# Performance work log

Hardware: AMD Instinct MI355X
Metric: run time of the kernel (lower is better)

Reference implementation:

```python
import jax, jax.numpy as jnp
import numpy as np

CHANS = [512, 1024, 512, 256, 256, 256]
RES = [(38, 38), (19, 19), (10, 10), (5, 5), (3, 3), (1, 1)]
NB = [4, 6, 6, 6, 4, 4]  # 2 + 2*len(aspect_ratios) per level (SSD300)
NC = 80                   # num_classes (conf conv outputs NC+1 per box)
B = 8


def _conv3x3(x, w, b):
    # x: [B, C, H, W], w: [O, C, 3, 3], stride 1, padding 1 (SAME)
    y = jax.lax.conv_general_dilated(
        x, w, window_strides=(1, 1), padding='SAME',
        dimension_numbers=('NCHW', 'OIHW', 'NCHW'))
    return y + b[None, :, None, None]


def setup_inputs() -> dict:
    key = jax.random.key(0)
    ks = jax.random.split(key, 6 * 3)
    d = {}
    for i in range(6):
        C = CHANS[i]
        H, W = RES[i]
        nb = NB[i]
        k = ks[i * 3:(i + 1) * 3]
        d[f'x{i}'] = jax.random.normal(k[0], (B, C, H, W), jnp.float32)
        d[f'loc_w{i}'] = jax.random.normal(k[1], (nb * 4, C, 3, 3), jnp.float32) * 0.02
        d[f'loc_b{i}'] = jnp.zeros((nb * 4,), jnp.float32)
        d[f'conf_w{i}'] = jax.random.normal(k[2], (nb * (NC + 1), C, 3, 3), jnp.float32) * 0.02
        d[f'conf_b{i}'] = jnp.zeros((nb * (NC + 1),), jnp.float32)
    return d


def reference(x0, loc_w0, loc_b0, conf_w0, conf_b0,
              x1, loc_w1, loc_b1, conf_w1, conf_b1,
              x2, loc_w2, loc_b2, conf_w2, conf_b2,
              x3, loc_w3, loc_b3, conf_w3, conf_b3,
              x4, loc_w4, loc_b4, conf_w4, conf_b4,
              x5, loc_w5, loc_b5, conf_w5, conf_b5):
    xs = [x0, x1, x2, x3, x4, x5]
    lws = [loc_w0, loc_w1, loc_w2, loc_w3, loc_w4, loc_w5]
    lbs = [loc_b0, loc_b1, loc_b2, loc_b3, loc_b4, loc_b5]
    cws = [conf_w0, conf_w1, conf_w2, conf_w3, conf_w4, conf_w5]
    cbs = [conf_b0, conf_b1, conf_b2, conf_b3, conf_b4, conf_b5]
    locs, confs = [], []
    for x, lw, lb, cw, cb in zip(xs, lws, lbs, cws, cbs):
        b = x.shape[0]
        # loc(act).view(B, 4, -1).permute(0, 2, 1)
        loc = _conv3x3(x, lw, lb).reshape(b, 4, -1).transpose(0, 2, 1)
        # conf(act).view(B, NC+1, -1).permute(0, 2, 1)
        conf = _conv3x3(x, cw, cb).reshape(b, NC + 1, -1).transpose(0, 2, 1)
        locs.append(loc)
        confs.append(conf)
    pred_locs = jnp.concatenate(locs, axis=1)    # [B, 8732, 4]
    pred_labels = jnp.concatenate(confs, axis=1)  # [B, 8732, 81]
    return pred_locs, pred_labels
```

## Files before the change

kernel.cpp:

```cpp
#include <hip/hip_runtime.h>
#include <stdint.h>


#define NTH 256
#define ATOT 8732
#define LOCTOT 279424
#define QS 36
#define TOTOUT 5937760
#define MR 8

typedef short short8 __attribute__((ext_vector_type(8)));
typedef float f32x4 __attribute__((ext_vector_type(4)));

__device__ __forceinline__ unsigned short f2bf(float f) {
  unsigned u = __float_as_uint(f);
  u += 0x7fffu + ((u >> 16) & 1u);
  return (unsigned short)(u >> 16);
}

__device__ __forceinline__ void gload_lds16(const void* g, void* l) {
  __builtin_amdgcn_global_load_lds(
      (const __attribute__((address_space(1))) unsigned int*)g,
      (__attribute__((address_space(3))) unsigned int*)l, 16, 0, 0);
}

struct PXs { const float* x; unsigned short* xh; int C, HWp, ptiles, boff; };
struct PX { PXs s[6]; };

__global__ __launch_bounds__(NTH) void prep_x(PX P) {
  __shared__ float T[64][65];
  const int bid = blockIdx.x;
  int e = 0;
  #pragma unroll
  for (int i = 1; i < 6; ++i) if (bid >= P.s[i].boff) e = i;
  const PXs sp = P.s[e];
  const int local = bid - sp.boff;
  const int p64 = local % sp.ptiles;
  const int t2  = local / sp.ptiles;
  const int Cq  = sp.C >> 6;
  const int c64 = t2 % Cq;
  const int bb  = t2 / Cq;

  const int tid = threadIdx.x;
  const int p0 = p64 << 6;
  const float* xs = sp.x + (size_t)(bb * sp.C + (c64 << 6)) * sp.HWp;
  const int tx = tid & 63, ty = tid >> 6;
  const int p = p0 + tx;
  const bool pok = p < sp.HWp;
  #pragma unroll
  for (int j = 0; j < 16; ++j) {
    int c = ty + (j << 2);
    T[c][tx] = pok ? xs[(size_t)c * sp.HWp + p] : 0.f;
  }
  __syncthreads();
  const int pl = tid >> 2, cs = (tid & 3) << 4;
  const int pg = p0 + pl;
  if (pg < sp.HWp) {
    unsigned short* dst = sp.xh + ((size_t)bb * sp.HWp + pg) * sp.C + (c64 << 6) + cs;
    short8 v0, v1;
    #pragma unroll
    for (int j = 0; j < 8; ++j) {
      v0[j] = (short)f2bf(T[cs + j][pl]);
      v1[j] = (short)f2bf(T[cs + 8 + j][pl]);
    }
    *(short8*)dst = v0;
    *(short8*)(dst + 8) = v1;
  }
}

struct PWs { const float *lw, *cw; unsigned short* wp; int C, lC, Nloc, Ntot, Npad, Kp; size_t tbase; };
struct PW { PWs s[6]; };

__global__ __launch_bounds__(NTH) void prep_w(PW P) {
  const size_t g = (size_t)blockIdx.x * NTH + threadIdx.x;
  int e = 0;
  #pragma unroll
  for (int i = 1; i < 6; ++i) if (g >= P.s[i].tbase) e = i;
  const PWs sp = P.s[e];
  const size_t local = g - sp.tbase;
  const int ci = (int)(local & (size_t)(sp.C - 1));
  const int co = (int)(local >> sp.lC);
  if (co >= sp.Npad) return;
  unsigned short* dst = sp.wp + (size_t)co * sp.Kp + ci;
  if (co >= sp.Ntot) {
    #pragma unroll
    for (int r = 0; r < 9; ++r) dst[(size_t)r * sp.C] = 0;
    return;
  }
  const float* wr = (co < sp.Nloc)
      ? (sp.lw + ((size_t)co * sp.C + ci) * 9)
      : (sp.cw + ((size_t)(co - sp.Nloc) * sp.C + ci) * 9);
  float v[9];
  #pragma unroll
  for (int r = 0; r < 9; ++r) v[r] = wr[r];
  #pragma unroll
  for (int r = 0; r < 9; ++r) dst[(size_t)r * sp.C] = f2bf(v[r]);
}

struct SG {
  const unsigned short *xh, *wp;
  float* yb;
  int H, W, HWp, C, lCq, Cq, Kp, M, Npad, mtiles, lgS, boff;
};
struct AG { SG s[6]; const char* zeros; int gq, gr; };

__global__ __launch_bounds__(NTH) void mbox_gemm(AG P) {
  __shared__ __align__(16) unsigned short A_s[2][128 * 64];
  __shared__ __align__(16) unsigned short B_s[2][128 * 64];

  const int bid = blockIdx.x;
  const int xcd = bid & 7, sidx = bid >> 3;
  const int g = (xcd < P.gr) ? xcd * (P.gq + 1) + sidx
                             : P.gr * (P.gq + 1) + (xcd - P.gr) * P.gq + sidx;

  int e = 0;
  #pragma unroll
  for (int i = 1; i < 6; ++i) if (g >= P.s[i].boff) e = i;
  const SG sp = P.s[e];
  const int gl = g - sp.boff;
  const int ks = gl & ((1 << sp.lgS) - 1);
  const int t2 = gl >> sp.lgS;
  const int mtile = t2 % sp.mtiles;
  const int ntile = t2 / sp.mtiles;

  const int tid = threadIdx.x, lane = tid & 63, wv = tid >> 6;
  const int wm = wv >> 1, wn = wv & 1;
  const int swz = ((lane & 7) ^ (lane >> 3)) << 4;
  const int rsub = lane >> 3;

  int bA[4], hA[4], wA[4]; bool mok[4];
  #pragma unroll
  for (int i = 0; i < 4; ++i) {
    int row = (wv << 5) + (i << 3) + rsub;
    int mg = mtile * 128 + row;
    bool ok = mg < sp.M;
    int mc = ok ? mg : 0;
    int bb = mc / sp.HWp; int p = mc - bb * sp.HWp;
    int hh = p / sp.W;    int ww = p - hh * sp.W;
    bA[i] = bb; hA[i] = hh; wA[i] = ww; mok[i] = ok;
  }

  const int q0 = ks * QS, q1 = q0 + QS;

  const char* curB[4];
  #pragma unroll
  for (int i = 0; i < 4; ++i) {
    int row = (wv << 5) + (i << 3) + rsub;
    int nrow = ntile * 128 + row;
    curB[i] = (const char*)(sp.wp + (size_t)nrow * sp.Kp + (size_t)q0 * 64) + swz;
  }

  const char* curA[4];
  auto setA = [&](int rr, int cq0) {
    int d3 = rr / 3; int dh = d3 - 1, dw = rr - d3 * 3 - 1;
    #pragma unroll
    for (int i = 0; i < 4; ++i) {
      int hh = hA[i] + dh, ww = wA[i] + dw;
      bool ok = mok[i] & ((unsigned)hh < (unsigned)sp.H) & ((unsigned)ww < (unsigned)sp.W);
      const unsigned short* base = ok
          ? sp.xh + (((size_t)bA[i] * sp.H + hh) * sp.W + ww) * sp.C + (cq0 << 6)
          : (const unsigned short*)P.zeros;
      curA[i] = (const char*)base + swz;
    }
  };

  auto stage = [&](int buf) {
    char* As = (char*)&A_s[buf][0];
    char* Bs = (char*)&B_s[buf][0];
    #pragma unroll
    for (int i = 0; i < 4; ++i)
      gload_lds16(curA[i], As + ((wv << 5) + (i << 3)) * 128);
    #pragma unroll
    for (int i = 0; i < 4; ++i)
      gload_lds16(curB[i], Bs + ((wv << 5) + (i << 3)) * 128);
  };

  f32x4 acc[4][4] = {};
  const int l15 = lane & 15, lh = lane >> 4;

  setA(q0 >> sp.lCq, q0 & (sp.Cq - 1));
  stage(0);
  #pragma unroll
  for (int i = 0; i < 4; ++i) { curA[i] += 128; curB[i] += 128; }

  int cur = 0;
  for (int q = q0; q < q1; ++q) {
    __syncthreads();
    if (q + 1 < q1) {
      if (((q + 1) & (sp.Cq - 1)) == 0) setA((q + 1) >> sp.lCq, 0);
      stage(cur ^ 1);
      #pragma unroll
      for (int i = 0; i < 4; ++i) { curA[i] += 128; curB[i] += 128; }
    }
    const char* As = (const char*)&A_s[cur][0];
    const char* Bs = (const char*)&B_s[cur][0];
    #pragma unroll
    for (int kk = 0; kk < 2; ++kk) {
      const int klb = ((kk << 5) + (lh << 3)) << 1;
      short8 af[4], bv[4];
      #pragma unroll
      for (int mf = 0; mf < 4; ++mf) {
        int row = (wm << 6) + (mf << 4) + l15;
        af[mf] = *(const short8*)(As + row * 128 + (klb ^ ((row & 7) << 4)));
      }
      #pragma unroll
      for (int nf = 0; nf < 4; ++nf) {
        int row = (wn << 6) + (nf << 4) + l15;
        bv[nf] = *(const short8*)(Bs + row * 128 + (klb ^ ((row & 7) << 4)));
      }
      #pragma unroll
      for (int mf = 0; mf < 4; ++mf)
        #pragma unroll
        for (int nf = 0; nf < 4; ++nf)
          acc[mf][nf] = __builtin_amdgcn_mfma_f32_16x16x32_bf16(af[mf], bv[nf], acc[mf][nf], 0, 0, 0);
    }
    cur ^= 1;
  }

  float* yb = sp.yb + (size_t)ks * sp.M * sp.Npad;
  #pragma unroll
  for (int nf = 0; nf < 4; ++nf) {
    const int ncol = ntile * 128 + (wn << 6) + (nf << 4) + l15;
    #pragma unroll
    for (int mf = 0; mf < 4; ++mf) {
      #pragma unroll
      for (int rg = 0; rg < 4; ++rg) {
        const int mg = mtile * 128 + (wm << 6) + (mf << 4) + (lh << 2) + rg;
        if (mg < sp.M) yb[(size_t)mg * sp.Npad + ncol] = acc[mf][nf][rg];
      }
    }
  }
}

struct SC2s { const float *yb, *lb, *cb; int HW, nb, S, Npad, M, abase, boff; };
struct SC2 { SC2s s[6]; };

__global__ __launch_bounds__(NTH) void mbox_scatter(SC2 P, float* __restrict__ out) {
  __shared__ float T[MR * 512];
  __shared__ float LB[32], CB[512];
  const int bid = blockIdx.x;
  int e = 0;
  #pragma unroll
  for (int i = 1; i < 6; ++i) if (bid >= P.s[i].boff) e = i;
  const SC2s sp = P.s[e];
  const int m0 = (bid - sp.boff) * MR;
  const int tid = threadIdx.x;
  const int HW = sp.HW, nb = sp.nb, Npad = sp.Npad;
  const int nb4v = nb * 4;

  for (int i = tid; i < nb4v; i += NTH) LB[i] = sp.lb[i];
  for (int i = tid; i < nb * 81; i += NTH) CB[i] = sp.cb[i];

  const int np4 = Npad >> 2;
  const int tot4 = MR * np4;
  const size_t dstride4 = (size_t)sp.M * np4;
  const float4* yb4 = (const float4*)sp.yb + (size_t)m0 * np4;
  float4* T4 = (float4*)T;
  for (int idx = tid; idx < tot4; idx += NTH) {
    const float4* p = yb4 + idx;
    float4 v = *p;
    for (int k = 1; k < sp.S; ++k) {
      p += dstride4;
      float4 w = *p;
      v.x += w.x; v.y += w.y; v.z += w.z; v.w += w.w;
    }
    T4[idx] = v;
  }
  __syncthreads();

  if (tid < MR * nb) {
    const int mloc = tid / nb, rb = tid - (tid / nb) * nb;
    const int m = m0 + mloc;
    const int b = m / HW, p = m - b * HW;
    const int aidx = sp.abase + rb * HW + p;
    float4 v;
    #pragma unroll
    for (int ii = 0; ii < 4; ++ii)
      (&v.x)[ii] = T[mloc * Npad + ii * nb + rb] + LB[ii * nb + rb];
    ((float4*)out)[(size_t)b * ATOT + aidx] = v;
  }

  const int totc = MR * nb * 81;
  float* outc = out + LOCTOT;
  for (int f = tid; f < totc; f += NTH) {
    const int ii = f % 81;
    const int gg = f / 81;
    const int rb = gg % nb;
    const int mloc = gg / nb;
    const int m = m0 + mloc;
    const int b = m / HW, p = m - b * HW;
    const int aidx = sp.abase + rb * HW + p;
    const int c = ii * nb + rb;
    outc[((size_t)b * ATOT + aidx) * 81 + ii] = T[mloc * Npad + nb4v + c] + CB[c];
  }
}

extern "C" void kernel_launch(void* const* d_in, const int* in_sizes, int n_in,
                              void* d_out, int out_size, void* d_ws, size_t ws_size,
                              hipStream_t stream) {
  static const int CH[6]  = {512, 1024, 512, 256, 256, 256};
  static const int HH[6]  = {38, 19, 10, 5, 3, 1};
  static const int NB_[6] = {4, 6, 6, 6, 4, 4};
  static const int SK[6]  = {2, 4, 2, 1, 1, 1};
  static const int LGS[6] = {1, 2, 1, 0, 0, 0};

  int abase[6]; { int a = 0; for (int s = 0; s < 6; ++s) { abase[s] = a; a += NB_[s] * HH[s] * HH[s]; } }

  size_t xh_off[6], wp_off[6], yb_off[6], off = 0;
  auto al = [](size_t v) { return (v + 255) & ~(size_t)255; };
  for (int s = 0; s < 6; ++s) { xh_off[s] = off; off = al(off + (size_t)8 * HH[s] * HH[s] * CH[s] * 2); }
  for (int s = 0; s < 6; ++s) {
    wp_off[s] = off;
    int Npad = ((NB_[s] * 85 + 127) / 128) * 128;
    off = al(off + (size_t)Npad * (CH[s] * 9) * 2);
  }
  const size_t zeros_off = off; off = al(off + 8192);
  for (int s = 0; s < 6; ++s) {
    yb_off[s] = off;
    int Npad = ((NB_[s] * 85 + 127) / 128) * 128;
    off = al(off + (size_t)SK[s] * (8 * HH[s] * HH[s]) * Npad * 4);
  }
  (void)ws_size;

  char* ws = (char*)d_ws;
  (void)hipMemsetAsync(ws + zeros_off, 0, 8192, stream);

  PX px; int pxb = 0;
  for (int s = 0; s < 6; ++s) {
    PXs& p = px.s[s];
    p.x = (const float*)d_in[5 * s + 0];
    p.xh = (unsigned short*)(ws + xh_off[s]);
    p.C = CH[s]; p.HWp = HH[s] * HH[s];
    p.ptiles = (p.HWp + 63) / 64;
    p.boff = pxb;
    pxb += 8 * (CH[s] >> 6) * p.ptiles;
  }
  hipLaunchKernelGGL(prep_x, dim3(pxb), dim3(NTH), 0, stream, px);

  PW pw; size_t tb = 0;
  for (int s = 0; s < 6; ++s) {
    PWs& p = pw.s[s];
    p.lw = (const float*)d_in[5 * s + 1];
    p.cw = (const float*)d_in[5 * s + 3];
    p.wp = (unsigned short*)(ws + wp_off[s]);
    p.C = CH[s];
    p.lC = (CH[s] == 1024) ? 10 : (CH[s] == 512 ? 9 : 8);
    p.Nloc = NB_[s] * 4; p.Ntot = NB_[s] * 85;
    p.Npad = ((p.Ntot + 127) / 128) * 128;
    p.Kp = CH[s] * 9;
    p.tbase = tb;
    tb += (size_t)p.Npad * CH[s];
  }
  hipLaunchKernelGGL(prep_w, dim3((unsigned)((tb + NTH - 1) / NTH)), dim3(NTH), 0, stream, pw);

  AG ag; ag.zeros = ws + zeros_off;
  int G = 0;
  for (int s = 0; s < 6; ++s) {
    SG& g = ag.s[s];
    g.xh = (const unsigned short*)(ws + xh_off[s]);
    g.wp = (const unsigned short*)(ws + wp_off[s]);
    g.yb = (float*)(ws + yb_off[s]);
    g.H = HH[s]; g.W = HH[s]; g.HWp = HH[s] * HH[s];
    g.C = CH[s];
    g.Cq = CH[s] >> 6;
    g.lCq = (g.Cq == 16) ? 4 : (g.Cq == 8 ? 3 : 2);
    g.Kp = CH[s] * 9;
    g.M = 8 * g.HWp;
    g.Npad = ((NB_[s] * 85 + 127) / 128) * 128;
    g.mtiles = (g.M + 127) / 128;
    g.lgS = LGS[s];
    g.boff = G;
    G += g.mtiles * (g.Npad >> 7) * SK[s];
  }
  ag.gq = G / 8; ag.gr = G % 8;
  hipLaunchKernelGGL(mbox_gemm, dim3(G), dim3(NTH), 0, stream, ag);

  SC2 sc; int SB = 0;
  for (int s = 0; s < 6; ++s) {
    SC2s& p = sc.s[s];
    p.yb = (const float*)(ws + yb_off[s]);
    p.lb = (const float*)d_in[5 * s + 2];
    p.cb = (const float*)d_in[5 * s + 4];
    p.HW = HH[s] * HH[s];
    p.nb = NB_[s];
    p.S = SK[s];
    p.Npad = ((NB_[s] * 85 + 127) / 128) * 128;
    p.M = 8 * p.HW;
    p.abase = abase[s];
    p.boff = SB;
    SB += p.M / MR;
  }
  hipLaunchKernelGGL(mbox_scatter, dim3(SB), dim3(NTH), 0, stream, sc, (float*)d_out);
}
```

Baseline: 148.3 us.

## Store GEMM split-K partials as bf16 and merge prep kernels into one launch

The GEMM now writes its split-K partial outputs as bf16 instead of fp32, halving the intermediate buffer traffic written by the GEMM and read back by the scatter kernel, which now sums bf16 partials in fp32. Separately, the activation-transpose and weight-repack prep kernels are fused into one launch that branches on block index, removing one kernel launch. The bf16 partials add rounding error to each split-K partial sum before the final reduction, which may affect output tolerance.

```diff
diff --git a/kernel.cpp b/kernel.cpp
--- a/kernel.cpp
+++ b/kernel.cpp
@@ -10,6 +10,7 @@
 #define MR 8
 
 typedef short short8 __attribute__((ext_vector_type(8)));
+typedef unsigned short ushort8 __attribute__((ext_vector_type(8)));
 typedef float f32x4 __attribute__((ext_vector_type(4)));
 
 __device__ __forceinline__ unsigned short f2bf(float f) {
@@ -18,6 +19,10 @@
   return (unsigned short)(u >> 16);
 }
 
+__device__ __forceinline__ float bf2f(unsigned short b) {
+  return __uint_as_float((unsigned)b << 16);
+}
+
 __device__ __forceinline__ void gload_lds16(const void* g, void* l) {
   __builtin_amdgcn_global_load_lds(
       (const __attribute__((address_space(1))) unsigned int*)g,
@@ -25,81 +30,79 @@
 }
 
 struct PXs { const float* x; unsigned short* xh; int C, HWp, ptiles, boff; };
-struct PX { PXs s[6]; };
-
-__global__ __launch_bounds__(NTH) void prep_x(PX P) {
+struct PWs { const float *lw, *cw; unsigned short* wp; int C, lC, Nloc, Ntot, Npad, Kp; size_t tbase; };
+struct PREP { PXs x[6]; PWs w[6]; int pxb; };
+
+__global__ __launch_bounds__(NTH) void prep_all(PREP P) {
   __shared__ float T[64][65];
-  const int bid = blockIdx.x;
-  int e = 0;
-  #pragma unroll
-  for (int i = 1; i < 6; ++i) if (bid >= P.s[i].boff) e = i;
-  const PXs sp = P.s[e];
-  const int local = bid - sp.boff;
-  const int p64 = local % sp.ptiles;
-  const int t2  = local / sp.ptiles;
-  const int Cq  = sp.C >> 6;
-  const int c64 = t2 % Cq;
-  const int bb  = t2 / Cq;
-
   const int tid = threadIdx.x;
-  const int p0 = p64 << 6;
-  const float* xs = sp.x + (size_t)(bb * sp.C + (c64 << 6)) * sp.HWp;
-  const int tx = tid & 63, ty = tid >> 6;
-  const int p = p0 + tx;
-  const bool pok = p < sp.HWp;
-  #pragma unroll
-  for (int j = 0; j < 16; ++j) {
-    int c = ty + (j << 2);
-    T[c][tx] = pok ? xs[(size_t)c * sp.HWp + p] : 0.f;
-  }
-  __syncthreads();
-  const int pl = tid >> 2, cs = (tid & 3) << 4;
-  const int pg = p0 + pl;
-  if (pg < sp.HWp) {
-    unsigned short* dst = sp.xh + ((size_t)bb * sp.HWp + pg) * sp.C + (c64 << 6) + cs;
-    short8 v0, v1;
-    #pragma unroll
-    for (int j = 0; j < 8; ++j) {
-      v0[j] = (short)f2bf(T[cs + j][pl]);
-      v1[j] = (short)f2bf(T[cs + 8 + j][pl]);
-    }
-    *(short8*)dst = v0;
-    *(short8*)(dst + 8) = v1;
-  }
-}
-
-struct PWs { const float *lw, *cw; unsigned short* wp; int C, lC, Nloc, Ntot, Npad, Kp; size_t tbase; };
-struct PW { PWs s[6]; };
-
-__global__ __launch_bounds__(NTH) void prep_w(PW P) {
-  const size_t g = (size_t)blockIdx.x * NTH + threadIdx.x;
-  int e = 0;
-  #pragma unroll
-  for (int i = 1; i < 6; ++i) if (g >= P.s[i].tbase) e = i;
-  const PWs sp = P.s[e];
-  const size_t local = g - sp.tbase;
-  const int ci = (int)(local & (size_t)(sp.C - 1));
-  const int co = (int)(local >> sp.lC);
-  if (co >= sp.Npad) return;
-  unsigned short* dst = sp.wp + (size_t)co * sp.Kp + ci;
-  if (co >= sp.Ntot) {
-    #pragma unroll
-    for (int r = 0; r < 9; ++r) dst[(size_t)r * sp.C] = 0;
-    return;
-  }
-  const float* wr = (co < sp.Nloc)
-      ? (sp.lw + ((size_t)co * sp.C + ci) * 9)
-      : (sp.cw + ((size_t)(co - sp.Nloc) * sp.C + ci) * 9);
-  float v[9];
-  #pragma unroll
-  for (int r = 0; r < 9; ++r) v[r] = wr[r];
-  #pragma unroll
-  for (int r = 0; r < 9; ++r) dst[(size_t)r * sp.C] = f2bf(v[r]);
+  if ((int)blockIdx.x < P.pxb) {
+    const int bid = blockIdx.x;
+    int e = 0;
+    #pragma unroll
+    for (int i = 1; i < 6; ++i) if (bid >= P.x[i].boff) e = i;
+    const PXs sp = P.x[e];
+    const int local = bid - sp.boff;
+    const int p64 = local % sp.ptiles;
+    const int t2  = local / sp.ptiles;
+    const int Cq  = sp.C >> 6;
+    const int c64 = t2 % Cq;
+    const int bb  = t2 / Cq;
+
+    const int p0 = p64 << 6;
+    const float* xs = sp.x + (size_t)(bb * sp.C + (c64 << 6)) * sp.HWp;
+    const int tx = tid & 63, ty = tid >> 6;
+    const int p = p0 + tx;
+    const bool pok = p < sp.HWp;
+    #pragma unroll
+    for (int j = 0; j < 16; ++j) {
+      int c = ty + (j << 2);
+      T[c][tx] = pok ? xs[(size_t)c * sp.HWp + p] : 0.f;
+    }
+    __syncthreads();
+    const int pl = tid >> 2, cs = (tid & 3) << 4;
+    const int pg = p0 + pl;
+    if (pg < sp.HWp) {
+      unsigned short* dst = sp.xh + ((size_t)bb * sp.HWp + pg) * sp.C + (c64 << 6) + cs;
+      short8 v0, v1;
+      #pragma unroll
+      for (int j = 0; j < 8; ++j) {
+        v0[j] = (short)f2bf(T[cs + j][pl]);
+        v1[j] = (short)f2bf(T[cs + 8 + j][pl]);
+      }
+      *(short8*)dst = v0;
+      *(short8*)(dst + 8) = v1;
+    }
+  } else {
+    const size_t g = (size_t)(blockIdx.x - P.pxb) * NTH + tid;
+    int e = 0;
+    #pragma unroll
+    for (int i = 1; i < 6; ++i) if (g >= P.w[i].tbase) e = i;
+    const PWs sp = P.w[e];
+    const size_t local = g - sp.tbase;
+    const int ci = (int)(local & (size_t)(sp.C - 1));
+    const int co = (int)(local >> sp.lC);
+    if (co >= sp.Npad) return;
+    unsigned short* dst = sp.wp + (size_t)co * sp.Kp + ci;
+    if (co >= sp.Ntot) {
+      #pragma unroll
+      for (int r = 0; r < 9; ++r) dst[(size_t)r * sp.C] = 0;
+      return;
+    }
+    const float* wr = (co < sp.Nloc)
+        ? (sp.lw + ((size_t)co * sp.C + ci) * 9)
+        : (sp.cw + ((size_t)(co - sp.Nloc) * sp.C + ci) * 9);
+    float v[9];
+    #pragma unroll
+    for (int r = 0; r < 9; ++r) v[r] = wr[r];
+    #pragma unroll
+    for (int r = 0; r < 9; ++r) dst[(size_t)r * sp.C] = f2bf(v[r]);
+  }
 }
 
 struct SG {
   const unsigned short *xh, *wp;
-  float* yb;
+  unsigned short* yb;
   int H, W, HWp, C, lCq, Cq, Kp, M, Npad, mtiles, lgS, boff;
 };
 struct AG { SG s[6]; const char* zeros; int gq, gr; };
@@ -217,7 +220,7 @@
     cur ^= 1;
   }
 
-  float* yb = sp.yb + (size_t)ks * sp.M * sp.Npad;
+  unsigned short* yb = sp.yb + (size_t)ks * sp.M * sp.Npad;
   #pragma unroll
   for (int nf = 0; nf < 4; ++nf) {
     const int ncol = ntile * 128 + (wn << 6) + (nf << 4) + l15;
@@ -226,13 +229,13 @@
       #pragma unroll
       for (int rg = 0; rg < 4; ++rg) {
         const int mg = mtile * 128 + (wm << 6) + (mf << 4) + (lh << 2) + rg;
-        if (mg < sp.M) yb[(size_t)mg * sp.Npad + ncol] = acc[mf][nf][rg];
+        if (mg < sp.M) yb[(size_t)mg * sp.Npad + ncol] = f2bf(acc[mf][nf][rg]);
       }
     }
   }
 }
 
-struct SC2s { const float *yb, *lb, *cb; int HW, nb, S, Npad, M, abase, boff; };
+struct SC2s { const unsigned short* yb; const float *lb, *cb; int HW, nb, S, Npad, M, abase, boff; };
 struct SC2 { SC2s s[6]; };
 
 __global__ __launch_bounds__(NTH) void mbox_scatter(SC2 P, float* __restrict__ out) {
@@ -251,20 +254,20 @@
   for (int i = tid; i < nb4v; i += NTH) LB[i] = sp.lb[i];
   for (int i = tid; i < nb * 81; i += NTH) CB[i] = sp.cb[i];
 
-  const int np4 = Npad >> 2;
-  const int tot4 = MR * np4;
-  const size_t dstride4 = (size_t)sp.M * np4;
-  const float4* yb4 = (const float4*)sp.yb + (size_t)m0 * np4;
-  float4* T4 = (float4*)T;
-  for (int idx = tid; idx < tot4; idx += NTH) {
-    const float4* p = yb4 + idx;
-    float4 v = *p;
-    for (int k = 1; k < sp.S; ++k) {
-      p += dstride4;
-      float4 w = *p;
-      v.x += w.x; v.y += w.y; v.z += w.z; v.w += w.w;
-    }
-    T4[idx] = v;
+  const int np8 = Npad >> 3;
+  const int tot8 = MR * np8;
+  const size_t dstride8 = (size_t)sp.M * np8;
+  const ushort8* yb8 = (const ushort8*)sp.yb + (size_t)m0 * np8;
+  for (int idx = tid; idx < tot8; idx += NTH) {
+    float v[8] = {0.f, 0.f, 0.f, 0.f, 0.f, 0.f, 0.f, 0.f};
+    const ushort8* p = yb8 + idx;
+    for (int k = 0; k < sp.S; ++k) {
+      ushort8 w = *p; p += dstride8;
+      #pragma unroll
+      for (int j = 0; j < 8; ++j) v[j] += bf2f(w[j]);
+    }
+    #pragma unroll
+    for (int j = 0; j < 8; ++j) T[(idx << 3) + j] = v[j];
   }
   __syncthreads();
 
@@ -318,16 +321,16 @@
   for (int s = 0; s < 6; ++s) {
     yb_off[s] = off;
     int Npad = ((NB_[s] * 85 + 127) / 128) * 128;
-    off = al(off + (size_t)SK[s] * (8 * HH[s] * HH[s]) * Npad * 4);
+    off = al(off + (size_t)SK[s] * (8 * HH[s] * HH[s]) * Npad * 2);
   }
   (void)ws_size;
 
   char* ws = (char*)d_ws;
   (void)hipMemsetAsync(ws + zeros_off, 0, 8192, stream);
 
-  PX px; int pxb = 0;
-  for (int s = 0; s < 6; ++s) {
-    PXs& p = px.s[s];
+  PREP pp; int pxb = 0;
+  for (int s = 0; s < 6; ++s) {
+    PXs& p = pp.x[s];
     p.x = (const float*)d_in[5 * s + 0];
     p.xh = (unsigned short*)(ws + xh_off[s]);
     p.C = CH[s]; p.HWp = HH[s] * HH[s];
@@ -335,11 +338,9 @@
     p.boff = pxb;
     pxb += 8 * (CH[s] >> 6) * p.ptiles;
   }
-  hipLaunchKernelGGL(prep_x, dim3(pxb), dim3(NTH), 0, stream, px);
-
-  PW pw; size_t tb = 0;
-  for (int s = 0; s < 6; ++s) {
-    PWs& p = pw.s[s];
+  size_t tb = 0;
+  for (int s = 0; s < 6; ++s) {
+    PWs& p = pp.w[s];
     p.lw = (const float*)d_in[5 * s + 1];
     p.cw = (const float*)d_in[5 * s + 3];
     p.wp = (unsigned short*)(ws + wp_off[s]);
@@ -351,7 +352,9 @@
     p.tbase = tb;
     tb += (size_t)p.Npad * CH[s];
   }
-  hipLaunchKernelGGL(prep_w, dim3((unsigned)((tb + NTH - 1) / NTH)), dim3(NTH), 0, stream, pw);
+  pp.pxb = pxb;
+  const int pwb = (int)((tb + NTH - 1) / NTH);
+  hipLaunchKernelGGL(prep_all, dim3(pxb + pwb), dim3(NTH), 0, stream, pp);
 
   AG ag; ag.zeros = ws + zeros_off;
   int G = 0;
@@ -359,7 +362,7 @@
     SG& g = ag.s[s];
     g.xh = (const unsigned short*)(ws + xh_off[s]);
     g.wp = (const unsigned short*)(ws + wp_off[s]);
-    g.yb = (float*)(ws + yb_off[s]);
+    g.yb = (unsigned short*)(ws + yb_off[s]);
     g.H = HH[s]; g.W = HH[s]; g.HWp = HH[s] * HH[s];
     g.C = CH[s];
     g.Cq = CH[s] >> 6;
@@ -378,7 +381,7 @@
   SC2 sc; int SB = 0;
   for (int s = 0; s < 6; ++s) {
     SC2s& p = sc.s[s];
-    p.yb = (const float*)(ws + yb_off[s]);
+    p.yb = (const unsigned short*)(ws + yb_off[s]);
     p.lb = (const float*)d_in[5 * s + 2];
     p.cb = (const float*)d_in[5 * s + 4];
     p.HW = HH[s] * HH[s];
```

New measurement: 138.3 us. 1.07x faster.
